# Optimization experiments

Hardware: AMD Instinct MI355X
Metric: run time of the kernel (lower is better)

The kernel has to match this reference:

```python
import jax, jax.numpy as jnp
import numpy as np

B = 8          # batch
K = 200        # tex_params (PCA components)
N_UV = 5023    # number of uv query points (FLAME vertex count)
V = 786432     # 512*512*3 flat texture size


def setup_inputs() -> dict:
    key = jax.random.key(0)
    k1, k2, k3, k4 = jax.random.split(key, 4)
    texcode = jax.random.normal(k1, (B, K), dtype=jnp.float32)
    uv_coords = jax.random.uniform(k2, (N_UV, 2), dtype=jnp.float32)
    texture_mean = jax.random.normal(k3, (1, 1, V), dtype=jnp.float32)
    texture_basis = jax.random.normal(k4, (1, V, K), dtype=jnp.float32) * 0.01
    return {
        "texcode": texcode,
        "uv_coords": uv_coords,
        "texture_mean": texture_mean,
        "texture_basis": texture_basis,
    }


def reference(texcode, uv_coords, texture_mean, texture_basis):
    # PCA linear combination: mean + basis @ texcode  (expressed as GEMM, not
    # a materialized (B, V, K) elementwise product)
    tex = texture_mean[0] + jnp.einsum("vk,bk->bv", texture_basis[0], texcode)  # (B, V)
    tex = tex.reshape(B, 512, 512, 3).transpose(0, 3, 1, 2)  # (B, 3, 512, 512)
    # F.interpolate(size=[256,256]) defaults to nearest: src index = floor(i*512/256) = 2i
    tex = tex[:, :, ::2, ::2]  # (B, 3, 256, 256)
    tex = tex[:, ::-1, :, :]   # channel reorder [2, 1, 0] (RGB -> BGR)
    x = jnp.clip((uv_coords[:, 0] * 256.0).astype(jnp.int32), 0, 255)
    y = jnp.clip(((1.0 - uv_coords[:, 1]) * 256.0).astype(jnp.int32), 0, 255)
    return tex[:, :, y, x]  # (B, 3, N_UV)
```

## Files before the change

### kernel.cpp

```cpp
#include <hip/hip_runtime.h>


#define B_SZ 8
#define K_SZ 200

__global__ __launch_bounds__(64) void flametex_sample_kernel(
    const float* __restrict__ texcode,
    const float* __restrict__ uv,
    const float* __restrict__ mean,
    const float* __restrict__ basis,
    float* __restrict__ out,
    int N)
{
    const int n    = blockIdx.x;
    const int c    = blockIdx.y;
    const int lane = threadIdx.x;

    const float u0 = uv[2 * n + 0];
    const float u1 = uv[2 * n + 1];
    int xi = (int)(u0 * 256.0f);
    xi = min(max(xi, 0), 255);
    int yi = (int)((1.0f - u1) * 256.0f);
    yi = min(max(yi, 0), 255);
    const int v = 3072 * yi + 6 * xi + (2 - c);

    const float* __restrict__ brow = basis + (long long)v * K_SZ;

    float partial[B_SZ];
#pragma unroll
    for (int b = 0; b < B_SZ; ++b) partial[b] = 0.0f;

    for (int k = lane; k < K_SZ; k += 64) {
        const float bk = brow[k];
#pragma unroll
        for (int b = 0; b < B_SZ; ++b)
            partial[b] += bk * texcode[b * K_SZ + k];
    }

    const float mv = mean[v];
#pragma unroll
    for (int b = 0; b < B_SZ; ++b) {
        float s = partial[b];
#pragma unroll
        for (int off = 32; off > 0; off >>= 1)
            s += __shfl_down(s, off, 64);
        if (lane == 0)
            out[((long long)b * 3 + c) * N + n] = mv + s;
    }
}

extern "C" void kernel_launch(void* const* d_in, const int* in_sizes, int n_in,
                              void* d_out, int out_size, void* d_ws, size_t ws_size,
                              hipStream_t stream) {
    const float* texcode = (const float*)d_in[0];
    const float* uv      = (const float*)d_in[1];
    const float* mean    = (const float*)d_in[2];
    const float* basis   = (const float*)d_in[3];
    float* out = (float*)d_out;

    const int N = in_sizes[1] / 2;

    dim3 grid(N, 3);
    flametex_sample_kernel<<<grid, 64, 0, stream>>>(texcode, uv, mean, basis, out, N);
}
```

Before: 680.9 us.

## Stage texcode in shared memory and remap lanes to (k-group, batch) pairs

Packs four (vertex, channel) pairs into each 256-thread block and loads the full texcode matrix into LDS once per block. Each lane now owns one batch index and a 25-element k-slice, so the 8-way reduction over batches becomes three xor shuffles instead of eight full 64-lane reductions. The cost is redundant per-block texcode staging plus a barrier, and basis reads become strided per lane (8 lanes share a row slice) rather than coalesced across 64 lanes.

```diff
diff --git a/kernel.cpp b/kernel.cpp
--- a/kernel.cpp
+++ b/kernel.cpp
@@ -3,8 +3,9 @@
 
 #define B_SZ 8
 #define K_SZ 200
+#define PAIRS_PER_BLOCK 4
 
-__global__ __launch_bounds__(64) void flametex_sample_kernel(
+__global__ __launch_bounds__(256) void flametex_sample_kernel(
     const float* __restrict__ texcode,
     const float* __restrict__ uv,
     const float* __restrict__ mean,
@@ -12,9 +13,23 @@
     float* __restrict__ out,
     int N)
 {
-    const int n    = blockIdx.x;
-    const int c    = blockIdx.y;
-    const int lane = threadIdx.x;
+    __shared__ float s_tex[B_SZ * K_SZ];
+
+    const int tid = threadIdx.x;
+
+    for (int i = tid; i < B_SZ * K_SZ; i += 256)
+        s_tex[i] = texcode[i];
+    __syncthreads();
+
+    const int p = blockIdx.x * PAIRS_PER_BLOCK + (tid >> 6);
+    if (p >= 3 * N) return;
+
+    const int n = p / 3;
+    const int c = p - 3 * n;
+
+    const int lane = tid & 63;
+    const int kg   = lane >> 3;
+    const int b    = lane & 7;
 
     const float u0 = uv[2 * n + 0];
     const float u1 = uv[2 * n + 1];
@@ -24,29 +39,20 @@
     yi = min(max(yi, 0), 255);
     const int v = 3072 * yi + 6 * xi + (2 - c);
 
-    const float* __restrict__ brow = basis + (long long)v * K_SZ;
+    const float* __restrict__ brow = basis + (long long)v * K_SZ + kg * 25;
+    const float* __restrict__ trow = s_tex + b * K_SZ + kg * 25;
 
-    float partial[B_SZ];
+    float acc = 0.0f;
 #pragma unroll
-    for (int b = 0; b < B_SZ; ++b) partial[b] = 0.0f;
+    for (int i = 0; i < 25; ++i)
+        acc += brow[i] * trow[i];
 
-    for (int k = lane; k < K_SZ; k += 64) {
-        const float bk = brow[k];
-#pragma unroll
-        for (int b = 0; b < B_SZ; ++b)
-            partial[b] += bk * texcode[b * K_SZ + k];
-    }
+    acc += __shfl_xor(acc, 8, 64);
+    acc += __shfl_xor(acc, 16, 64);
+    acc += __shfl_xor(acc, 32, 64);
 
-    const float mv = mean[v];
-#pragma unroll
-    for (int b = 0; b < B_SZ; ++b) {
-        float s = partial[b];
-#pragma unroll
-        for (int off = 32; off > 0; off >>= 1)
-            s += __shfl_down(s, off, 64);
-        if (lane == 0)
-            out[((long long)b * 3 + c) * N + n] = mv + s;
-    }
+    if (kg == 0)
+        out[((long long)b * 3 + c) * N + n] = mean[v] + acc;
 }
 
 extern "C" void kernel_launch(void* const* d_in, const int* in_sizes, int n_in,
@@ -59,7 +65,8 @@
     float* out = (float*)d_out;
 
     const int N = in_sizes[1] / 2;
+    const int total = 3 * N;
+    const int blocks = (total + PAIRS_PER_BLOCK - 1) / PAIRS_PER_BLOCK;
 
-    dim3 grid(N, 3);
-    flametex_sample_kernel<<<grid, 64, 0, stream>>>(texcode, uv, mean, basis, out, N);
+    flametex_sample_kernel<<<blocks, 256, 0, stream>>>(texcode, uv, mean, basis, out, N);
 }
```

Measured after the change: 669.8 us. No clear change (-1.6%).
